# Optimization experiments

Hardware: AMD Instinct MI355X
Metric: run time of the kernel (lower is better)

## Reference

```python
import jax, jax.numpy as jnp
import numpy as np

N = 50000   # nodes per graph stream
E = 800000  # edges per graph stream
G = 100     # graphs in batch
FIN, H = 74, 256


def setup_inputs() -> dict:
    key = jax.random.key(0)
    ks = jax.random.split(key, 16)
    d = {
        'xl': jax.random.normal(ks[0], (N, FIN), jnp.float32),
        'xr': jax.random.normal(ks[1], (N, FIN), jnp.float32),
        'src_l': jax.random.randint(ks[2], (E,), 0, N, jnp.int32),
        'dst_l': jax.random.randint(ks[3], (E,), 0, N, jnp.int32),
        'src_r': jax.random.randint(ks[4], (E,), 0, N, jnp.int32),
        'dst_r': jax.random.randint(ks[5], (E,), 0, N, jnp.int32),
        'gid_l': jnp.sort(jax.random.randint(ks[6], (N,), 0, G, jnp.int32)),
        'gid_r': jnp.sort(jax.random.randint(ks[7], (N,), 0, G, jnp.int32)),
        'W0': jax.random.normal(ks[8], (FIN, H), jnp.float32) / np.sqrt(FIN),
        'b0': jnp.zeros((H,), jnp.float32),
        'W1': jax.random.normal(ks[9], (H, H), jnp.float32) / np.sqrt(H),
        'b1': jnp.zeros((H,), jnp.float32),
        'W2': jax.random.normal(ks[10], (H, H), jnp.float32) / np.sqrt(H),
        'b2': jnp.zeros((H,), jnp.float32),
        'Wf1': jax.random.normal(ks[11], (2 * H, H), jnp.float32) / np.sqrt(2 * H),
        'bf1': jnp.zeros((H,), jnp.float32),
        'Wf2': jax.random.normal(ks[12], (H, 1), jnp.float32) / np.sqrt(H),
        'bf2': jnp.zeros((1,), jnp.float32),
    }
    return d


def _deg_isqrt(idx, n):
    deg = jax.ops.segment_sum(jnp.ones_like(idx, jnp.float32), idx, num_segments=n)
    return jax.lax.rsqrt(jnp.maximum(deg, 1.0))


def _graph_conv(x, src, dst, do_isq, di_isq, W, b):
    # DGL GraphConv, norm='both': h = relu(D_in^{-1/2} A D_out^{-1/2} X W + b)
    h = (x * do_isq[:, None]) @ W            # transform-first (in_feats >= out for layer0 path is fine mathematically)
    agg = jax.ops.segment_sum(h[src], dst, num_segments=x.shape[0])
    return jax.nn.relu(agg * di_isq[:, None] + b)


def reference(xl, xr, src_l, dst_l, src_r, dst_r, gid_l, gid_r,
              W0, b0, W1, b1, W2, b2, Wf1, bf1, Wf2, bf2):
    do_l, di_l = _deg_isqrt(src_l, N), _deg_isqrt(dst_l, N)
    do_r, di_r = _deg_isqrt(src_r, N), _deg_isqrt(dst_r, N)
    Ws, bs = (W0, W1, W2), (b0, b1, b2)
    hl, hr = xl, xr
    for W, b in zip(Ws, bs):  # shared weights across both graph streams
        hl = _graph_conv(hl, src_l, dst_l, do_l, di_l, W, b)
        hr = _graph_conv(hr, src_r, dst_r, do_r, di_r, W, b)
    pl = jax.ops.segment_sum(hl, gid_l, num_segments=G)  # dgl.sum_nodes
    pr = jax.ops.segment_sum(hr, gid_r, num_segments=G)
    z = jnp.concatenate([pl, pr], axis=-1)               # [G, 2H]
    return jax.nn.relu(z @ Wf1 + bf1) @ Wf2 + bf2        # [G, 1]
```

## Files before the change

### kernel.cpp

```cpp
#include <hip/hip_runtime.h>

#define N_NODES 50000
#define N_EDGES 800000
#define N_GRAPHS 100
#define FIN_DIM 74
#define K0 96
#define H_DIM 256
#define EG 3125
#define XS_BLKS 18750
#define WCONV_BLKS 608
#define AGG0_BLKS 3128
#define AGGH_BLKS 6256
#define GEMM_BLKS 782
#define POOL_BLKS 782
#define SCAN_BLOCKS 196

typedef float f32x4 __attribute__((ext_vector_type(4)));
typedef unsigned int u32x4 __attribute__((ext_vector_type(4)));
typedef unsigned short us8 __attribute__((ext_vector_type(8)));
typedef __bf16 bf16x8 __attribute__((ext_vector_type(8)));

__device__ __forceinline__ unsigned short f2bf(float x) {
    unsigned u = __builtin_bit_cast(unsigned, x);
    u += 0x7fff + ((u >> 16) & 1);
    return (unsigned short)(u >> 16);
}
__device__ __forceinline__ float bf2f(unsigned short h) {
    return __builtin_bit_cast(float, (unsigned)h << 16);
}
__device__ __forceinline__ void acc8(float* a, us8 v) {
    u32x4 w = __builtin_bit_cast(u32x4, v);
    #pragma unroll
    for (int i = 0; i < 4; ++i) {
        a[2 * i]     += __builtin_bit_cast(float, w[i] << 16);
        a[2 * i + 1] += __builtin_bit_cast(float, w[i] & 0xffff0000u);
    }
}


__device__ __forceinline__ void hist_body(int bid, const int* __restrict__ src,
                                          const int* __restrict__ dst,
                                          int* __restrict__ cs, int* __restrict__ fc,
                                          int* __restrict__ rk) {
    int e = bid * 256 + threadIdx.x;
    if (e < N_EDGES) {
        rk[e] = atomicAdd(&fc[dst[e]], 1);
        atomicAdd(&cs[src[e]], 1);
    }
}

__device__ __forceinline__ void scat_body(int bid, const int* __restrict__ src,
                                          const int* __restrict__ dst,
                                          const int* __restrict__ rp,
                                          const int* __restrict__ rk,
                                          int* __restrict__ col) {
    int e = bid * 256 + threadIdx.x;
    if (e < N_EDGES) {
        int d = dst[e];
        col[rp[d] + rk[e]] = src[e];
    }
}

__device__ __forceinline__ void xscale_body(int bid, const float* __restrict__ x,
                                            const float* __restrict__ dso,
                                            unsigned short* __restrict__ xp) {
    int id = bid * 256 + threadIdx.x;
    int n = id / 96, f = id - n * 96;
    float v = (f < FIN_DIM) ? x[(size_t)n * FIN_DIM + f] * dso[n] : 0.f;
    xp[(size_t)(f >> 4) * (N_NODES * 16) + (size_t)n * 16 + (f & 15)] = f2bf(v);
}

__device__ __forceinline__ void wconv_body(int bid, const float* __restrict__ W0,
                                           const float* __restrict__ W1,
                                           const float* __restrict__ W2,
                                           unsigned short* __restrict__ Wt) {
    int id = bid * 256 + threadIdx.x;
    if (id < 256 * 96) {
        int n = id / 96, k = id - n * 96;
        float v = (k < FIN_DIM) ? W0[(size_t)k * H_DIM + n] : 0.f;
        Wt[id] = f2bf(v);
    } else if (id < 256 * 96 + 65536) {
        int id2 = id - 256 * 96;
        int n = id2 >> 8, k = id2 & 255;
        Wt[id] = f2bf(W1[(size_t)k * H_DIM + n]);
    } else {
        int id3 = id - 256 * 96 - 65536;
        int n = id3 >> 8, k = id3 & 255;
        Wt[id] = f2bf(W2[(size_t)k * H_DIM + n]);
    }
}

template<int SW, int NACT, int NSL>
__device__ __forceinline__ void agg_body(int abid, int cg,
                                         const unsigned short* __restrict__ h,
                                         const int* __restrict__ rp,
                                         const int* __restrict__ col,
                                         unsigned short* __restrict__ A) {
    const int CPB = SW / 8;
    const int NPB = 256 / CPB;
    if (cg >= NSL) return;
    int slot = threadIdx.x & (CPB - 1);
    int n = (abid >> 3) * NPB + threadIdx.x / CPB;
    if (n >= N_NODES) return;
    unsigned short* dst = A + (size_t)cg * (N_NODES * SW) + (size_t)n * SW + slot * 8;
    if (cg >= NACT) { us8 z = {}; *(us8*)dst = z; return; }
    const unsigned short* hs = h + (size_t)cg * (N_NODES * SW) + slot * 8;
    int beg = rp[n], end = rp[n + 1];
    float a[8] = {};
    int j = beg;
    for (; j + 3 < end; j += 4) {
        int s0 = col[j], s1 = col[j + 1], s2 = col[j + 2], s3 = col[j + 3];
        us8 v0 = *(const us8*)(hs + (size_t)s0 * SW);
        us8 v1 = *(const us8*)(hs + (size_t)s1 * SW);
        us8 v2 = *(const us8*)(hs + (size_t)s2 * SW);
        us8 v3 = *(const us8*)(hs + (size_t)s3 * SW);
        acc8(a, v0); acc8(a, v1); acc8(a, v2); acc8(a, v3);
    }
    for (; j < end; ++j)
        acc8(a, *(const us8*)(hs + (size_t)col[j] * SW));
    us8 r;
    #pragma unroll
    for (int i = 0; i < 8; ++i) r[i] = f2bf(a[i]);
    *(us8*)dst = r;
}

__device__ __forceinline__ void pool_body(int nb, const unsigned short* __restrict__ h,
                                          const int* __restrict__ gid,
                                          float* __restrict__ pool) {
    int n0 = nb * 64;
    int f = threadIdx.x;
    const unsigned short* hf = h + (size_t)(f >> 5) * (N_NODES * 32) + (f & 31);
    int end = min(n0 + 64, N_NODES);
    float acc = 0.0f;
    int gcur = gid[n0];
    for (int i = n0; i < end; ++i) {
        int g = gid[i];
        if (g != gcur) {
            atomicAdd(&pool[(size_t)gcur * H_DIM + f], acc);
            acc = 0.0f;
            gcur = g;
        }
        acc += bf2f(hf[(size_t)i * 32]);
    }
    atomicAdd(&pool[(size_t)gcur * H_DIM + f], acc);
}

template<int K, int SW>
__device__ __forceinline__ void gemm_body(int id, const unsigned short* __restrict__ A,
                                          const unsigned short* __restrict__ Wt,
                                          const float* __restrict__ bias,
                                          const float* __restrict__ dsi,
                                          const float* __restrict__ scale,
                                          unsigned short* __restrict__ C,
                                          unsigned short* smem) {
    unsigned short (*Ah)[40] = (unsigned short(*)[40])smem;
    unsigned short (*Bh)[40] = (unsigned short(*)[40])(smem + 128 * 40);
    const int M = N_NODES;

    int tid = threadIdx.x;
    int lane = tid & 63, wid = tid >> 6;
    int wm = (wid >> 1) * 64, wn = (wid & 1) * 64;
    int bm = (id >> 1) * 128, bn = (id & 1) * 128;

    f32x4 acc[4][4] = {};
    int r0 = wm + (lane & 15);
    int c0 = wn + (lane & 15);
    int kA = (lane >> 4) * 8;

    for (int k0 = 0; k0 < K; k0 += 32) {
        #pragma unroll
        for (int i = 0; i < 2; ++i) {
            int q = tid + i * 256;
            int row = q >> 2, k8 = (q & 3) * 8;
            int gm = bm + row;
            int kk = k0 + k8;
            us8 v = {};
            if (gm < M)
                v = *(const us8*)(A + (size_t)(kk / SW) * ((size_t)N_NODES * SW)
                                    + (size_t)gm * SW + (kk % SW));
            *(us8*)&Ah[row][k8] = v;
        }
        {
            int colx = tid & 127, kg = tid >> 7;
            const unsigned short* wsrc = Wt + (size_t)(bn + colx) * K + k0 + kg * 16;
            us8 w0 = *(const us8*)(wsrc);
            us8 w1 = *(const us8*)(wsrc + 8);
            *(us8*)&Bh[colx][kg * 16] = w0;
            *(us8*)&Bh[colx][kg * 16 + 8] = w1;
        }
        __syncthreads();

        bf16x8 ah[4], bh[4];
        #pragma unroll
        for (int m = 0; m < 4; ++m)
            ah[m] = __builtin_bit_cast(bf16x8, *(const us8*)&Ah[r0 + m * 16][kA]);
        #pragma unroll
        for (int n = 0; n < 4; ++n)
            bh[n] = __builtin_bit_cast(bf16x8, *(const us8*)&Bh[c0 + n * 16][kA]);

        #pragma unroll
        for (int m = 0; m < 4; ++m)
            #pragma unroll
            for (int n = 0; n < 4; ++n)
                acc[m][n] = __builtin_amdgcn_mfma_f32_16x16x32_bf16(ah[m], bh[n], acc[m][n], 0, 0, 0);
        __syncthreads();
    }

    int rowq = (lane >> 4) * 4;
    #pragma unroll
    for (int n = 0; n < 4; ++n) {
        int gn = bn + wn + n * 16 + (lane & 15);
        float bv = bias[gn];
        unsigned short* cs = C + (size_t)(gn >> 5) * (N_NODES * 32) + (gn & 31);
        #pragma unroll
        for (int m = 0; m < 4; ++m) {
            #pragma unroll
            for (int j = 0; j < 4; ++j) {
                int gm = bm + wm + m * 16 + rowq + j;
                if (gm < M) {
                    float r = fmaxf(acc[m][n][j] * dsi[gm] + bv, 0.0f);
                    if (scale) r *= scale[gm];
                    cs[(size_t)gm * 32] = f2bf(r);
                }
            }
        }
    }
}


__device__ __forceinline__ int block_excl_scan(int v, int* wsums) {
    int lane = threadIdx.x & 63, w = threadIdx.x >> 6;
    int x = v;
    #pragma unroll
    for (int ofs = 1; ofs < 64; ofs <<= 1) {
        int y = __shfl_up(x, ofs, 64);
        if (lane >= ofs) x += y;
    }
    if (lane == 63) wsums[w] = x;
    __syncthreads();
    int wo = 0;
    #pragma unroll
    for (int k = 0; k < 4; ++k) if (k < w) wo += wsums[k];
    return wo + x - v;
}

__global__ void k_whist(const float* __restrict__ W0, const float* __restrict__ W1,
                        const float* __restrict__ W2, unsigned short* __restrict__ Wt,
                        const int* __restrict__ src, const int* __restrict__ dst,
                        int* __restrict__ cs, int* __restrict__ fc, int* __restrict__ rk) {
    int bid = blockIdx.x;
    if (bid < WCONV_BLKS) wconv_body(bid, W0, W1, W2, Wt);
    else                  hist_body(bid - WCONV_BLKS, src, dst, cs, fc, rk);
}

__global__ void deg_scan1_kernel(const int* __restrict__ cs, const int* __restrict__ fc,
                                 float* __restrict__ dso, float* __restrict__ dsi,
                                 int* __restrict__ rp, int* __restrict__ bs) {
    __shared__ int ws[4];
    int i = blockIdx.x * 256 + threadIdx.x;
    int v = 0;
    if (i < N_NODES) {
        dso[i] = rsqrtf(fmaxf((float)cs[i], 1.0f));
        v = fc[i];
        dsi[i] = rsqrtf(fmaxf((float)v, 1.0f));
    }
    int ex = block_excl_scan(v, ws);
    if (i < N_NODES) rp[i] = ex;
    if (threadIdx.x == 255) bs[blockIdx.x] = ex + v;
}

__global__ void scan2_kernel(int* __restrict__ bs, int nb) {
    __shared__ int ws[4];
    int i = threadIdx.x;
    int v = (i < nb) ? bs[i] : 0;
    int ex = block_excl_scan(v, ws);
    __syncthreads();
    if (i < nb) bs[i] = ex;
}

__global__ void scan3_kernel(int* __restrict__ rp, const int* __restrict__ bs) {
    int i = blockIdx.x * 256 + threadIdx.x;
    if (i < N_NODES) rp[i] += bs[blockIdx.x];
    if (i == 0) rp[N_NODES] = N_EDGES;
}

__global__ void fuse_hsx(const int* __restrict__ srcR, const int* __restrict__ dstR,
                         int* __restrict__ csR, int* __restrict__ fcR, int* __restrict__ rkR,
                         const int* __restrict__ srcL, const int* __restrict__ dstL,
                         const int* __restrict__ rpL, const int* __restrict__ rkL,
                         int* __restrict__ colL,
                         const float* __restrict__ xL, const float* __restrict__ dsoL,
                         unsigned short* __restrict__ xpL) {
    int bid = blockIdx.x;
    if (bid < EG)            hist_body(bid, srcR, dstR, csR, fcR, rkR);
    else if (bid < 2 * EG)   scat_body(bid - EG, srcL, dstL, rpL, rkL, colL);
    else                     xscale_body(bid - 2 * EG, xL, dsoL, xpL);
}

__global__ void fuse_dsagg0(const int* __restrict__ csR, const int* __restrict__ fcR,
                            float* __restrict__ dsoR, float* __restrict__ dsiR,
                            int* __restrict__ rpR, int* __restrict__ bsR,
                            const unsigned short* __restrict__ xpL, const int* __restrict__ rpL,
                            const int* __restrict__ colL, unsigned short* __restrict__ AL) {
    __shared__ int ws[4];
    int bid = blockIdx.x;
    if (bid < SCAN_BLOCKS) {
        int i = bid * 256 + threadIdx.x;
        int v = 0;
        if (i < N_NODES) {
            dsoR[i] = rsqrtf(fmaxf((float)csR[i], 1.0f));
            v = fcR[i];
            dsiR[i] = rsqrtf(fmaxf((float)v, 1.0f));
        }
        int ex = block_excl_scan(v, ws);
        if (i < N_NODES) rpR[i] = ex;
        if (threadIdx.x == 255) bsR[bid] = ex + v;
    } else {
        agg_body<16, 5, 6>(bid - SCAN_BLOCKS, blockIdx.x & 7, xpL, rpL, colL, AL);
    }
}

__global__ void fuse_sxagg(const int* __restrict__ srcR, const int* __restrict__ dstR,
                           const int* __restrict__ rpR, const int* __restrict__ rkR,
                           int* __restrict__ colR,
                           const float* __restrict__ xR, const float* __restrict__ dsoR,
                           unsigned short* __restrict__ xpR,
                           const unsigned short* __restrict__ hL, const int* __restrict__ rpL,
                           const int* __restrict__ colL, unsigned short* __restrict__ AL) {
    int bid = blockIdx.x;
    if (bid < EG)                    scat_body(bid, srcR, dstR, rpR, rkR, colR);
    else if (bid < EG + XS_BLKS)     xscale_body(bid - EG, xR, dsoR, xpR);
    else agg_body<32, 8, 8>(bid - EG - XS_BLKS, blockIdx.x & 7, hL, rpL, colL, AL);
}

__global__ void fuse_agg_agg(const unsigned short* __restrict__ hL, const int* __restrict__ rpL,
                             const int* __restrict__ colL, unsigned short* __restrict__ AL,
                             const unsigned short* __restrict__ xpR, const int* __restrict__ rpR,
                             const int* __restrict__ colR, unsigned short* __restrict__ AR) {
    int bid = blockIdx.x;
    if (bid < AGGH_BLKS) agg_body<32, 8, 8>(bid, blockIdx.x & 7, hL, rpL, colL, AL);
    else agg_body<16, 5, 6>(bid - AGGH_BLKS, blockIdx.x & 7, xpR, rpR, colR, AR);
}

__global__ void fuse_pool_agg(const unsigned short* __restrict__ hP, const int* __restrict__ gidP,
                              float* __restrict__ poolP,
                              const unsigned short* __restrict__ hA, const int* __restrict__ rpA,
                              const int* __restrict__ colA, unsigned short* __restrict__ outA) {
    int bid = blockIdx.x;
    if (bid < POOL_BLKS) pool_body(bid, hP, gidP, poolP);
    else agg_body<32, 8, 8>(bid - POOL_BLKS, blockIdx.x & 7, hA, rpA, colA, outA);
}

template<int K, int SW>
__global__ __launch_bounds__(256) void gemm_kernel(
        const unsigned short* __restrict__ A, const unsigned short* __restrict__ Wt,
        const float* __restrict__ bias, const float* __restrict__ dsi,
        const float* __restrict__ scale, unsigned short* __restrict__ C) {
    __shared__ unsigned short smem[2 * 128 * 40];
    gemm_body<K, SW>(blockIdx.x, A, Wt, bias, dsi, scale, C, smem);
}

__global__ __launch_bounds__(256) void gemm_pair_kernel(
        const unsigned short* __restrict__ A1, const unsigned short* __restrict__ Wt2,
        const float* __restrict__ b2_, const float* __restrict__ dsi1, unsigned short* __restrict__ C1,
        const unsigned short* __restrict__ A2, const unsigned short* __restrict__ Wt0,
        const float* __restrict__ b0_, const float* __restrict__ dsi2,
        const float* __restrict__ sc2, unsigned short* __restrict__ C2) {
    __shared__ unsigned short smem[2 * 128 * 40];
    int bid = blockIdx.x;
    if (bid < GEMM_BLKS) gemm_body<H_DIM, 32>(bid, A1, Wt2, b2_, dsi1, nullptr, C1, smem);
    else                 gemm_body<K0, 16>(bid - GEMM_BLKS, A2, Wt0, b0_, dsi2, sc2, C2, smem);
}

__global__ void agg_kernel(const unsigned short* __restrict__ h, const int* __restrict__ rp,
                           const int* __restrict__ col, unsigned short* __restrict__ A) {
    agg_body<32, 8, 8>(blockIdx.x, blockIdx.x & 7, h, rp, col, A);
}

__global__ void pool_kernel(const unsigned short* __restrict__ h, const int* __restrict__ gid,
                            float* __restrict__ pool) {
    pool_body(blockIdx.x, h, gid, pool);
}

__global__ __launch_bounds__(256) void mlp_kernel(
        const float* __restrict__ pl, const float* __restrict__ pr,
        const float* __restrict__ Wf1, const float* __restrict__ bf1,
        const float* __restrict__ Wf2, const float* __restrict__ bf2,
        float* __restrict__ out) {
    __shared__ float z[512];
    __shared__ float red[256];
    int g = blockIdx.x, tid = threadIdx.x;
    z[tid] = pl[(size_t)g * H_DIM + tid];
    z[tid + 256] = pr[(size_t)g * H_DIM + tid];
    __syncthreads();
    float t = bf1[tid];
    #pragma unroll 8
    for (int k = 0; k < 512; ++k) t += z[k] * Wf1[(size_t)k * H_DIM + tid];
    t = fmaxf(t, 0.0f);
    red[tid] = t * Wf2[tid];
    __syncthreads();
    for (int ofs = 128; ofs > 0; ofs >>= 1) {
        if (tid < ofs) red[tid] += red[tid + ofs];
        __syncthreads();
    }
    if (tid == 0) out[g] = red[0] + bf2[0];
}


extern "C" void kernel_launch(void* const* d_in, const int* in_sizes, int n_in,
                              void* d_out, int out_size, void* d_ws, size_t ws_size,
                              hipStream_t stream) {
    const float* xl   = (const float*)d_in[0];
    const float* xr   = (const float*)d_in[1];
    const int* src_l  = (const int*)d_in[2];
    const int* dst_l  = (const int*)d_in[3];
    const int* src_r  = (const int*)d_in[4];
    const int* dst_r  = (const int*)d_in[5];
    const int* gid_l  = (const int*)d_in[6];
    const int* gid_r  = (const int*)d_in[7];
    const float* W0   = (const float*)d_in[8];
    const float* b0   = (const float*)d_in[9];
    const float* W1   = (const float*)d_in[10];
    const float* b1   = (const float*)d_in[11];
    const float* W2   = (const float*)d_in[12];
    const float* b2   = (const float*)d_in[13];
    const float* Wf1  = (const float*)d_in[14];
    const float* bf1  = (const float*)d_in[15];
    const float* Wf2  = (const float*)d_in[16];
    const float* bf2  = (const float*)d_in[17];
    float* out = (float*)d_out;
    (void)in_sizes; (void)n_in; (void)out_size; (void)ws_size;

    size_t off = 0;
    auto carve = [&](size_t bytes) {
        void* p = (char*)d_ws + off;
        off += (bytes + 255) & ~(size_t)255;
        return p;
    };
    const size_t NB4 = (size_t)N_NODES * 4;

    char* zstart = (char*)d_ws;
    int*   cs_l   = (int*)carve(NB4);
    int*   fc_l   = (int*)carve(NB4);
    int*   cs_r   = (int*)carve(NB4);
    int*   fc_r   = (int*)carve(NB4);
    float* pool_l = (float*)carve((size_t)N_GRAPHS * H_DIM * 4);
    float* pool_r = (float*)carve((size_t)N_GRAPHS * H_DIM * 4);
    size_t zbytes = off;

    float* dso_l = (float*)carve(NB4);
    float* dsi_l = (float*)carve(NB4);
    float* dso_r = (float*)carve(NB4);
    float* dsi_r = (float*)carve(NB4);
    int*   rp_l  = (int*)carve((size_t)(N_NODES + 1) * 4);
    int*   rp_r  = (int*)carve((size_t)(N_NODES + 1) * 4);
    int*   col_l = (int*)carve((size_t)N_EDGES * 4);
    int*   col_r = (int*)carve((size_t)N_EDGES * 4);
    int*   rk_l  = (int*)carve((size_t)N_EDGES * 4);
    int*   rk_r  = (int*)carve((size_t)N_EDGES * 4);
    int*   bs_l  = (int*)carve((size_t)SCAN_BLOCKS * 4);
    int*   bs_r  = (int*)carve((size_t)SCAN_BLOCKS * 4);

    unsigned short* Wt    = (unsigned short*)carve((size_t)(256 * 96 + 2 * 65536) * 2);
    unsigned short* Wt0   = Wt;
    unsigned short* Wt1   = Wt + 256 * 96;
    unsigned short* Wt2   = Wt + 256 * 96 + 65536;
    unsigned short* xp_l  = (unsigned short*)carve((size_t)N_NODES * 96 * 2);
    unsigned short* xp_r  = (unsigned short*)carve((size_t)N_NODES * 96 * 2);
    unsigned short* bufA_l = (unsigned short*)carve((size_t)N_NODES * H_DIM * 2);
    unsigned short* bufA_r = (unsigned short*)carve((size_t)N_NODES * H_DIM * 2);
    unsigned short* bufH_l = (unsigned short*)carve((size_t)N_NODES * H_DIM * 2);
    unsigned short* bufH_r = (unsigned short*)carve((size_t)N_NODES * H_DIM * 2);

    hipMemsetAsync(zstart, 0, zbytes, stream);

    k_whist<<<WCONV_BLKS + EG, 256, 0, stream>>>(W0, W1, W2, Wt,
                                                 src_l, dst_l, cs_l, fc_l, rk_l);
    deg_scan1_kernel<<<SCAN_BLOCKS, 256, 0, stream>>>(cs_l, fc_l, dso_l, dsi_l, rp_l, bs_l);
    scan2_kernel<<<1, 256, 0, stream>>>(bs_l, SCAN_BLOCKS);
    scan3_kernel<<<SCAN_BLOCKS, 256, 0, stream>>>(rp_l, bs_l);

    fuse_hsx<<<2 * EG + XS_BLKS, 256, 0, stream>>>(
        src_r, dst_r, cs_r, fc_r, rk_r,
        src_l, dst_l, rp_l, rk_l, col_l,
        xl, dso_l, xp_l);

    fuse_dsagg0<<<SCAN_BLOCKS + AGG0_BLKS, 256, 0, stream>>>(
        cs_r, fc_r, dso_r, dsi_r, rp_r, bs_r,
        xp_l, rp_l, col_l, bufA_l);
    scan2_kernel<<<1, 256, 0, stream>>>(bs_r, SCAN_BLOCKS);
    scan3_kernel<<<SCAN_BLOCKS, 256, 0, stream>>>(rp_r, bs_r);

    gemm_kernel<K0, 16><<<GEMM_BLKS, 256, 0, stream>>>(bufA_l, Wt0, b0, dsi_l, dso_l, bufH_l);

    fuse_sxagg<<<EG + XS_BLKS + AGGH_BLKS, 256, 0, stream>>>(
        src_r, dst_r, rp_r, rk_r, col_r,
        xr, dso_r, xp_r,
        bufH_l, rp_l, col_l, bufA_l);

    gemm_kernel<H_DIM, 32><<<GEMM_BLKS, 256, 0, stream>>>(bufA_l, Wt1, b1, dsi_l, dso_l, bufH_l);

    fuse_agg_agg<<<AGGH_BLKS + AGG0_BLKS, 256, 0, stream>>>(
        bufH_l, rp_l, col_l, bufA_l,
        xp_r, rp_r, col_r, bufA_r);

    gemm_pair_kernel<<<2 * GEMM_BLKS, 256, 0, stream>>>(
        bufA_l, Wt2, b2, dsi_l, bufH_l,
        bufA_r, Wt0, b0, dsi_r, dso_r, bufH_r);

    fuse_pool_agg<<<POOL_BLKS + AGGH_BLKS, 256, 0, stream>>>(
        bufH_l, gid_l, pool_l,
        bufH_r, rp_r, col_r, bufA_r);

    gemm_kernel<H_DIM, 32><<<GEMM_BLKS, 256, 0, stream>>>(bufA_r, Wt1, b1, dsi_r, dso_r, bufH_r);

    agg_kernel<<<AGGH_BLKS, 256, 0, stream>>>(bufH_r, rp_r, col_r, bufA_r);
    gemm_kernel<H_DIM, 32><<<GEMM_BLKS, 256, 0, stream>>>(bufA_r, Wt2, b2, dsi_r, nullptr, bufH_r);
    pool_kernel<<<POOL_BLKS, 256, 0, stream>>>(bufH_r, gid_r, pool_r);

    mlp_kernel<<<N_GRAPHS, 256, 0, stream>>>(pool_l, pool_r, Wf1, bf1, Wf2, bf2, out);
}
```

Baseline: 757.2 us.

## Process left and right graph streams in lockstep with paired kernel launches

Replaces the staggered, skewed pipeline, where the right stream lagged the left by one stage, with a lockstep schedule. Each stage now launches one kernel that covers both streams: the histogram, the scans via blockIdx.y, scatter plus x-scaling, aggregation, GEMM and pooling. This cuts the launch count and makes each launch uniform and larger. In exchange it gives up the earlier overlap of different kernel types, for example agg blocks running alongside scan or pool blocks.

```diff
diff --git a/kernel.cpp b/kernel.cpp
--- a/kernel.cpp
+++ b/kernel.cpp
@@ -244,18 +244,30 @@
     return wo + x - v;
 }
 
-__global__ void k_whist(const float* __restrict__ W0, const float* __restrict__ W1,
+__global__ void k_hist2(const float* __restrict__ W0, const float* __restrict__ W1,
                         const float* __restrict__ W2, unsigned short* __restrict__ Wt,
-                        const int* __restrict__ src, const int* __restrict__ dst,
-                        int* __restrict__ cs, int* __restrict__ fc, int* __restrict__ rk) {
+                        const int* __restrict__ srcL, const int* __restrict__ dstL,
+                        int* __restrict__ csL, int* __restrict__ fcL, int* __restrict__ rkL,
+                        const int* __restrict__ srcR, const int* __restrict__ dstR,
+                        int* __restrict__ csR, int* __restrict__ fcR, int* __restrict__ rkR) {
     int bid = blockIdx.x;
-    if (bid < WCONV_BLKS) wconv_body(bid, W0, W1, W2, Wt);
-    else                  hist_body(bid - WCONV_BLKS, src, dst, cs, fc, rk);
-}
-
-__global__ void deg_scan1_kernel(const int* __restrict__ cs, const int* __restrict__ fc,
-                                 float* __restrict__ dso, float* __restrict__ dsi,
-                                 int* __restrict__ rp, int* __restrict__ bs) {
+    if (bid < WCONV_BLKS)           wconv_body(bid, W0, W1, W2, Wt);
+    else if (bid < WCONV_BLKS + EG) hist_body(bid - WCONV_BLKS, srcL, dstL, csL, fcL, rkL);
+    else                            hist_body(bid - WCONV_BLKS - EG, srcR, dstR, csR, fcR, rkR);
+}
+
+__global__ void deg_scan1_kernel(const int* __restrict__ csL, const int* __restrict__ fcL,
+                                 float* __restrict__ dsoL, float* __restrict__ dsiL,
+                                 int* __restrict__ rpL, int* __restrict__ bsL,
+                                 const int* __restrict__ csR, const int* __restrict__ fcR,
+                                 float* __restrict__ dsoR, float* __restrict__ dsiR,
+                                 int* __restrict__ rpR, int* __restrict__ bsR) {
+    const int* cs = blockIdx.y ? csR : csL;
+    const int* fc = blockIdx.y ? fcR : fcL;
+    float* dso = blockIdx.y ? dsoR : dsoL;
+    float* dsi = blockIdx.y ? dsiR : dsiL;
+    int* rp = blockIdx.y ? rpR : rpL;
+    int* bs = blockIdx.y ? bsR : bsL;
     __shared__ int ws[4];
     int i = blockIdx.x * 256 + threadIdx.x;
     int v = 0;
@@ -269,7 +281,8 @@
     if (threadIdx.x == 255) bs[blockIdx.x] = ex + v;
 }
 
-__global__ void scan2_kernel(int* __restrict__ bs, int nb) {
+__global__ void scan2_kernel(int* __restrict__ bsL, int* __restrict__ bsR, int nb) {
+    int* bs = blockIdx.y ? bsR : bsL;
     __shared__ int ws[4];
     int i = threadIdx.x;
     int v = (i < nb) ? bs[i] : 0;
@@ -278,108 +291,65 @@
     if (i < nb) bs[i] = ex;
 }
 
-__global__ void scan3_kernel(int* __restrict__ rp, const int* __restrict__ bs) {
+__global__ void scan3_kernel(int* __restrict__ rpL, const int* __restrict__ bsL,
+                             int* __restrict__ rpR, const int* __restrict__ bsR) {
+    int* rp = blockIdx.y ? rpR : rpL;
+    const int* bs = blockIdx.y ? bsR : bsL;
     int i = blockIdx.x * 256 + threadIdx.x;
     if (i < N_NODES) rp[i] += bs[blockIdx.x];
     if (i == 0) rp[N_NODES] = N_EDGES;
 }
 
-__global__ void fuse_hsx(const int* __restrict__ srcR, const int* __restrict__ dstR,
-                         int* __restrict__ csR, int* __restrict__ fcR, int* __restrict__ rkR,
-                         const int* __restrict__ srcL, const int* __restrict__ dstL,
-                         const int* __restrict__ rpL, const int* __restrict__ rkL,
-                         int* __restrict__ colL,
-                         const float* __restrict__ xL, const float* __restrict__ dsoL,
-                         unsigned short* __restrict__ xpL) {
+__global__ void fuse_ssxx(const int* __restrict__ srcL, const int* __restrict__ dstL,
+                          const int* __restrict__ rpL, const int* __restrict__ rkL,
+                          int* __restrict__ colL,
+                          const int* __restrict__ srcR, const int* __restrict__ dstR,
+                          const int* __restrict__ rpR, const int* __restrict__ rkR,
+                          int* __restrict__ colR,
+                          const float* __restrict__ xL, const float* __restrict__ dsoL,
+                          unsigned short* __restrict__ xpL,
+                          const float* __restrict__ xR, const float* __restrict__ dsoR,
+                          unsigned short* __restrict__ xpR) {
     int bid = blockIdx.x;
-    if (bid < EG)            hist_body(bid, srcR, dstR, csR, fcR, rkR);
-    else if (bid < 2 * EG)   scat_body(bid - EG, srcL, dstL, rpL, rkL, colL);
-    else                     xscale_body(bid - 2 * EG, xL, dsoL, xpL);
-}
-
-__global__ void fuse_dsagg0(const int* __restrict__ csR, const int* __restrict__ fcR,
-                            float* __restrict__ dsoR, float* __restrict__ dsiR,
-                            int* __restrict__ rpR, int* __restrict__ bsR,
-                            const unsigned short* __restrict__ xpL, const int* __restrict__ rpL,
-                            const int* __restrict__ colL, unsigned short* __restrict__ AL) {
-    __shared__ int ws[4];
+    if (bid < EG)                         scat_body(bid, srcL, dstL, rpL, rkL, colL);
+    else if (bid < 2 * EG)                scat_body(bid - EG, srcR, dstR, rpR, rkR, colR);
+    else if (bid < 2 * EG + XS_BLKS)      xscale_body(bid - 2 * EG, xL, dsoL, xpL);
+    else                                  xscale_body(bid - 2 * EG - XS_BLKS, xR, dsoR, xpR);
+}
+
+template<int SW, int NACT, int NSL, int NB>
+__global__ void fuse_agg2(const unsigned short* __restrict__ hL, const int* __restrict__ rpL,
+                          const int* __restrict__ colL, unsigned short* __restrict__ AL,
+                          const unsigned short* __restrict__ hR, const int* __restrict__ rpR,
+                          const int* __restrict__ colR, unsigned short* __restrict__ AR) {
     int bid = blockIdx.x;
-    if (bid < SCAN_BLOCKS) {
-        int i = bid * 256 + threadIdx.x;
-        int v = 0;
-        if (i < N_NODES) {
-            dsoR[i] = rsqrtf(fmaxf((float)csR[i], 1.0f));
-            v = fcR[i];
-            dsiR[i] = rsqrtf(fmaxf((float)v, 1.0f));
-        }
-        int ex = block_excl_scan(v, ws);
-        if (i < N_NODES) rpR[i] = ex;
-        if (threadIdx.x == 255) bsR[bid] = ex + v;
-    } else {
-        agg_body<16, 5, 6>(bid - SCAN_BLOCKS, blockIdx.x & 7, xpL, rpL, colL, AL);
-    }
-}
-
-__global__ void fuse_sxagg(const int* __restrict__ srcR, const int* __restrict__ dstR,
-                           const int* __restrict__ rpR, const int* __restrict__ rkR,
-                           int* __restrict__ colR,
-                           const float* __restrict__ xR, const float* __restrict__ dsoR,
-                           unsigned short* __restrict__ xpR,
-                           const unsigned short* __restrict__ hL, const int* __restrict__ rpL,
-                           const int* __restrict__ colL, unsigned short* __restrict__ AL) {
-    int bid = blockIdx.x;
-    if (bid < EG)                    scat_body(bid, srcR, dstR, rpR, rkR, colR);
-    else if (bid < EG + XS_BLKS)     xscale_body(bid - EG, xR, dsoR, xpR);
-    else agg_body<32, 8, 8>(bid - EG - XS_BLKS, blockIdx.x & 7, hL, rpL, colL, AL);
-}
-
-__global__ void fuse_agg_agg(const unsigned short* __restrict__ hL, const int* __restrict__ rpL,
-                             const int* __restrict__ colL, unsigned short* __restrict__ AL,
-                             const unsigned short* __restrict__ xpR, const int* __restrict__ rpR,
-                             const int* __restrict__ colR, unsigned short* __restrict__ AR) {
-    int bid = blockIdx.x;
-    if (bid < AGGH_BLKS) agg_body<32, 8, 8>(bid, blockIdx.x & 7, hL, rpL, colL, AL);
-    else agg_body<16, 5, 6>(bid - AGGH_BLKS, blockIdx.x & 7, xpR, rpR, colR, AR);
-}
-
-__global__ void fuse_pool_agg(const unsigned short* __restrict__ hP, const int* __restrict__ gidP,
-                              float* __restrict__ poolP,
-                              const unsigned short* __restrict__ hA, const int* __restrict__ rpA,
-                              const int* __restrict__ colA, unsigned short* __restrict__ outA) {
-    int bid = blockIdx.x;
-    if (bid < POOL_BLKS) pool_body(bid, hP, gidP, poolP);
-    else agg_body<32, 8, 8>(bid - POOL_BLKS, blockIdx.x & 7, hA, rpA, colA, outA);
+    if (bid < NB) agg_body<SW, NACT, NSL>(bid, bid & 7, hL, rpL, colL, AL);
+    else {
+        int lb = bid - NB;
+        agg_body<SW, NACT, NSL>(lb, lb & 7, hR, rpR, colR, AR);
+    }
 }
 
 template<int K, int SW>
-__global__ __launch_bounds__(256) void gemm_kernel(
-        const unsigned short* __restrict__ A, const unsigned short* __restrict__ Wt,
-        const float* __restrict__ bias, const float* __restrict__ dsi,
-        const float* __restrict__ scale, unsigned short* __restrict__ C) {
-    __shared__ unsigned short smem[2 * 128 * 40];
-    gemm_body<K, SW>(blockIdx.x, A, Wt, bias, dsi, scale, C, smem);
-}
-
-__global__ __launch_bounds__(256) void gemm_pair_kernel(
-        const unsigned short* __restrict__ A1, const unsigned short* __restrict__ Wt2,
-        const float* __restrict__ b2_, const float* __restrict__ dsi1, unsigned short* __restrict__ C1,
-        const unsigned short* __restrict__ A2, const unsigned short* __restrict__ Wt0,
-        const float* __restrict__ b0_, const float* __restrict__ dsi2,
-        const float* __restrict__ sc2, unsigned short* __restrict__ C2) {
+__global__ __launch_bounds__(256) void gemm_pair2(
+        const unsigned short* __restrict__ AL, const float* __restrict__ dsiL,
+        const float* __restrict__ scL, unsigned short* __restrict__ CL,
+        const unsigned short* __restrict__ AR, const float* __restrict__ dsiR,
+        const float* __restrict__ scR, unsigned short* __restrict__ CR,
+        const unsigned short* __restrict__ Wt, const float* __restrict__ bias) {
     __shared__ unsigned short smem[2 * 128 * 40];
     int bid = blockIdx.x;
-    if (bid < GEMM_BLKS) gemm_body<H_DIM, 32>(bid, A1, Wt2, b2_, dsi1, nullptr, C1, smem);
-    else                 gemm_body<K0, 16>(bid - GEMM_BLKS, A2, Wt0, b0_, dsi2, sc2, C2, smem);
-}
-
-__global__ void agg_kernel(const unsigned short* __restrict__ h, const int* __restrict__ rp,
-                           const int* __restrict__ col, unsigned short* __restrict__ A) {
-    agg_body<32, 8, 8>(blockIdx.x, blockIdx.x & 7, h, rp, col, A);
-}
-
-__global__ void pool_kernel(const unsigned short* __restrict__ h, const int* __restrict__ gid,
-                            float* __restrict__ pool) {
-    pool_body(blockIdx.x, h, gid, pool);
+    if (bid < GEMM_BLKS) gemm_body<K, SW>(bid, AL, Wt, bias, dsiL, scL, CL, smem);
+    else                 gemm_body<K, SW>(bid - GEMM_BLKS, AR, Wt, bias, dsiR, scR, CR, smem);
+}
+
+__global__ void pool2_kernel(const unsigned short* __restrict__ hL, const int* __restrict__ gidL,
+                             float* __restrict__ poolL,
+                             const unsigned short* __restrict__ hR, const int* __restrict__ gidR,
+                             float* __restrict__ poolR) {
+    int bid = blockIdx.x;
+    if (bid < POOL_BLKS) pool_body(bid, hL, gidL, poolL);
+    else                 pool_body(bid - POOL_BLKS, hR, gidR, poolR);
 }
 
 __global__ __launch_bounds__(256) void mlp_kernel(
@@ -474,49 +444,49 @@
 
     hipMemsetAsync(zstart, 0, zbytes, stream);
 
-    k_whist<<<WCONV_BLKS + EG, 256, 0, stream>>>(W0, W1, W2, Wt,
-                                                 src_l, dst_l, cs_l, fc_l, rk_l);
-    deg_scan1_kernel<<<SCAN_BLOCKS, 256, 0, stream>>>(cs_l, fc_l, dso_l, dsi_l, rp_l, bs_l);
-    scan2_kernel<<<1, 256, 0, stream>>>(bs_l, SCAN_BLOCKS);
-    scan3_kernel<<<SCAN_BLOCKS, 256, 0, stream>>>(rp_l, bs_l);
-
-    fuse_hsx<<<2 * EG + XS_BLKS, 256, 0, stream>>>(
-        src_r, dst_r, cs_r, fc_r, rk_r,
+    k_hist2<<<WCONV_BLKS + 2 * EG, 256, 0, stream>>>(
+        W0, W1, W2, Wt,
+        src_l, dst_l, cs_l, fc_l, rk_l,
+        src_r, dst_r, cs_r, fc_r, rk_r);
+
+    deg_scan1_kernel<<<dim3(SCAN_BLOCKS, 2), 256, 0, stream>>>(
+        cs_l, fc_l, dso_l, dsi_l, rp_l, bs_l,
+        cs_r, fc_r, dso_r, dsi_r, rp_r, bs_r);
+    scan2_kernel<<<dim3(1, 2), 256, 0, stream>>>(bs_l, bs_r, SCAN_BLOCKS);
+    scan3_kernel<<<dim3(SCAN_BLOCKS, 2), 256, 0, stream>>>(rp_l, bs_l, rp_r, bs_r);
+
+    fuse_ssxx<<<2 * EG + 2 * XS_BLKS, 256, 0, stream>>>(
         src_l, dst_l, rp_l, rk_l, col_l,
-        xl, dso_l, xp_l);
-
-    fuse_dsagg0<<<SCAN_BLOCKS + AGG0_BLKS, 256, 0, stream>>>(
-        cs_r, fc_r, dso_r, dsi_r, rp_r, bs_r,
-        xp_l, rp_l, col_l, bufA_l);
-    scan2_kernel<<<1, 256, 0, stream>>>(bs_r, SCAN_BLOCKS);
-    scan3_kernel<<<SCAN_BLOCKS, 256, 0, stream>>>(rp_r, bs_r);
-
-    gemm_kernel<K0, 16><<<GEMM_BLKS, 256, 0, stream>>>(bufA_l, Wt0, b0, dsi_l, dso_l, bufH_l);
-
-    fuse_sxagg<<<EG + XS_BLKS + AGGH_BLKS, 256, 0, stream>>>(
         src_r, dst_r, rp_r, rk_r, col_r,
-        xr, dso_r, xp_r,
-        bufH_l, rp_l, col_l, bufA_l);
-
-    gemm_kernel<H_DIM, 32><<<GEMM_BLKS, 256, 0, stream>>>(bufA_l, Wt1, b1, dsi_l, dso_l, bufH_l);
-
-    fuse_agg_agg<<<AGGH_BLKS + AGG0_BLKS, 256, 0, stream>>>(
+        xl, dso_l, xp_l,
+        xr, dso_r, xp_r);
+
+    fuse_agg2<16, 5, 6, AGG0_BLKS><<<2 * AGG0_BLKS, 256, 0, stream>>>(
+        xp_l, rp_l, col_l, bufA_l,
+        xp_r, rp_r, col_r, bufA_r);
+    gemm_pair2<K0, 16><<<2 * GEMM_BLKS, 256, 0, stream>>>(
+        bufA_l, dsi_l, dso_l, bufH_l,
+        bufA_r, dsi_r, dso_r, bufH_r,
+        Wt0, b0);
+
+    fuse_agg2<32, 8, 8, AGGH_BLKS><<<2 * AGGH_BLKS, 256, 0, stream>>>(
         bufH_l, rp_l, col_l, bufA_l,
-        xp_r, rp_r, col_r, bufA_r);
-
-    gemm_pair_kernel<<<2 * GEMM_BLKS, 256, 0, stream>>>(
-        bufA_l, Wt2, b2, dsi_l, bufH_l,
-        bufA_r, Wt0, b0, dsi_r, dso_r, bufH_r);
-
-    fuse_pool_agg<<<POOL_BLKS + AGGH_BLKS, 256, 0, stream>>>(
+        bufH_r, rp_r, col_r, bufA_r);
+    gemm_pair2<H_DIM, 32><<<2 * GEMM_BLKS, 256, 0, stream>>>(
+        bufA_l, dsi_l, dso_l, bufH_l,
+        bufA_r, dsi_r, dso_r, bufH_r,
+        Wt1, b1);
+
+    fuse_agg2<32, 8, 8, AGGH_BLKS><<<2 * AGGH_BLKS, 256, 0, stream>>>(
+        bufH_l, rp_l, col_l, bufA_l,
+        bufH_r, rp_r, col_r, bufA_r);
+    gemm_pair2<H_DIM, 32><<<2 * GEMM_BLKS, 256, 0, stream>>>(
+        bufA_l, dsi_l, nullptr, bufH_l,
+        bufA_r, dsi_r, nullptr, bufH_r,
+        Wt2, b2);
+
+    pool2_kernel<<<2 * POOL_BLKS, 256, 0, stream>>>(
         bufH_l, gid_l, pool_l,
-        bufH_r, rp_r, col_r, bufA_r);
-
-    gemm_kernel<H_DIM, 32><<<GEMM_BLKS, 256, 0, stream>>>(bufA_r, Wt1, b1, dsi_r, dso_r, bufH_r);
-
-    agg_kernel<<<AGGH_BLKS, 256, 0, stream>>>(bufH_r, rp_r, col_r, bufA_r);
-    gemm_kernel<H_DIM, 32><<<GEMM_BLKS, 256, 0, stream>>>(bufA_r, Wt2, b2, dsi_r, nullptr, bufH_r);
-    pool_kernel<<<POOL_BLKS, 256, 0, stream>>>(bufH_r, gid_r, pool_r);
-
+        bufH_r, gid_r, pool_r);
     mlp_kernel<<<N_GRAPHS, 256, 0, stream>>>(pool_l, pool_r, Wf1, bf1, Wf2, bf2, out);
 }
```

Result: no change. 747.6 us (-1.3%).
